# Optimization experiments

Hardware: AMD Instinct MI355X
Metric: run time of the kernel (lower is better)

Reference implementation:

```python
import jax, jax.numpy as jnp
import numpy as np

VOCAB = 12149
EMB = 50
TAGS = 9
HID = 128
START = 7
B, T = 256, 512


def setup_inputs() -> dict:
    key = jax.random.key(0)
    ks = jax.random.split(key, 12)
    s = 0.05
    return {
        "inputs": jax.random.randint(ks[0], (B, T), 0, VOCAB),
        "seq_label": jax.random.randint(ks[1], (B, T), 0, TAGS),
        "emb": jax.random.normal(ks[2], (VOCAB, EMB), jnp.float32) * s,
        "enc_Wx": jax.random.normal(ks[3], (EMB, HID), jnp.float32) * s,
        "enc_Wh": jax.random.normal(ks[4], (HID, HID), jnp.float32) * s,
        "enc_b": jnp.zeros((HID,), jnp.float32),
        "dec_emb": jax.random.normal(ks[5], (TAGS, EMB), jnp.float32) * s,
        "dec_Wx": jax.random.normal(ks[6], (EMB, HID), jnp.float32) * s,
        "dec_Wh": jax.random.normal(ks[7], (HID, HID), jnp.float32) * s,
        "dec_b": jnp.zeros((HID,), jnp.float32),
        "W": jax.random.normal(ks[8], (HID, TAGS), jnp.float32) * s,
        "b": jnp.zeros((TAGS,), jnp.float32),
    }


def _rnn(x_tbd, h0, Wx, Wh, b, collect):
    # x_tbd: [T, B, E]; SimpleRNN cell: h_t = tanh(x_t Wx + h_{t-1} Wh + b)
    def step(h, xt):
        h = jnp.tanh(xt @ Wx + h @ Wh + b)
        return h, (h if collect else None)
    hT, hs = jax.lax.scan(step, h0, x_tbd)
    return hT, hs


def reference(inputs, seq_label, emb, enc_Wx, enc_Wh, enc_b,
              dec_emb, dec_Wx, dec_Wh, dec_b, W, b):
    Bsz = inputs.shape[0]
    h0 = jnp.zeros((Bsz, HID), jnp.float32)
    # Encoder: only the final state is used as the decoder's initial state
    x = emb[inputs]                                  # [B, T, EMB]
    state, _ = _rnn(jnp.swapaxes(x, 0, 1), h0, enc_Wx, enc_Wh, enc_b, False)
    # Teacher forcing: prepend START token, drop last label
    dec_in = jnp.concatenate(
        [jnp.full((Bsz, 1), START, seq_label.dtype), seq_label], axis=1)[:, :-1]
    dx = dec_emb[dec_in]                             # [B, T, EMB]
    _, hs = _rnn(jnp.swapaxes(dx, 0, 1), state, dec_Wx, dec_Wh, dec_b, True)
    hs = jnp.swapaxes(hs, 0, 1)                      # [B, T, HID]
    return hs @ W + b                                # [B, T, TAGS]
```

## Files before the change

### kernel.cpp

```cpp
#include <hip/hip_runtime.h>
#include <hip/hip_bf16.h>

#define VOCAB 12149
#define EMB 50
#define TAGS 9
#define HID 128
#define START_TOK 7
#define BSZ 256
#define TLEN 512

typedef float v2f __attribute__((ext_vector_type(2)));

__device__ __forceinline__ float tanh_fast(float x) {
  float e = __expf(2.0f * x);
  return 1.0f - 2.0f * __builtin_amdgcn_rcpf(e + 1.0f);
}

template<int CTRL>
__device__ __forceinline__ float dpp_mov(float x) {
  return __int_as_float(__builtin_amdgcn_update_dpp(
      0, __float_as_int(x), CTRL, 0xF, 0xF, true));
}
template<int CTRL>
__device__ __forceinline__ v2f dpp2(v2f x) {
  v2f r;
  r.x = dpp_mov<CTRL>(x.x);
  r.y = dpp_mov<CTRL>(x.y);
  return r;
}
#define DPP_XOR1 0xB1
#define DPP_XOR2 0x4E
#define DPP_ROR4 0x124
#define DPP_ROR8 0x128
#define DPP_HALF_MIRROR 0x141
#define DPP_MIRROR 0x140

__global__ __launch_bounds__(128) void exw_kernel(
    const float* __restrict__ emb, const float* __restrict__ Wx,
    const float* __restrict__ bv, float* __restrict__ exw)
{
  __shared__ float wx_s[EMB * HID];
  __shared__ float emb_s[8 * EMB];
  const int tid = threadIdx.x;
  const int v0 = blockIdx.x * 8;
  for (int idx = tid; idx < EMB * HID; idx += 128) wx_s[idx] = Wx[idx];
  for (int idx = tid; idx < 8 * EMB; idx += 128) {
    int r = idx / EMB;
    int e = idx - r * EMB;
    int v = v0 + r;
    emb_s[idx] = (v < VOCAB) ? emb[v * EMB + e] : 0.0f;
  }
  __syncthreads();
  const float bj = bv[tid];
  for (int r = 0; r < 8; ++r) {
    int v = v0 + r;
    if (v >= VOCAB) break;
    float acc = bj;
#pragma unroll
    for (int e = 0; e < EMB; ++e) acc += emb_s[r * EMB + e] * wx_s[e * HID + tid];
    exw[v * HID + tid] = acc;
  }
}

__device__ __forceinline__ void dot_step(const float4 hA, const float4 hB,
                                         const v2f* __restrict__ wv, v2f acc[4]) {
  const float ha[4] = {hA.x, hA.y, hA.z, hA.w};
  const float hb[4] = {hB.x, hB.y, hB.z, hB.w};
#pragma unroll
  for (int c = 0; c < 4; ++c) {
    v2f h2 = {ha[c], ha[c]};
#pragma unroll
    for (int m = 0; m < 4; ++m)
      acc[m] = __builtin_elementwise_fma(h2, wv[c * 4 + m], acc[m]);
  }
#pragma unroll
  for (int c = 0; c < 4; ++c) {
    v2f h2 = {hb[c], hb[c]};
#pragma unroll
    for (int m = 0; m < 4; ++m)
      acc[m] = __builtin_elementwise_fma(h2, wv[16 + c * 4 + m], acc[m]);
  }
}

__global__ __launch_bounds__(256) void rnn_kernel(
    const int* __restrict__ inputs, const int* __restrict__ labels,
    const float* __restrict__ exw,
    const float* __restrict__ encWh,
    const float* __restrict__ dembG, const float* __restrict__ decWx,
    const float* __restrict__ decWh, const float* __restrict__ decb,
    const float* __restrict__ W, const float* __restrict__ bout,
    float* __restrict__ out)
{
  __shared__ __align__(16) float h_s[2][HID];
  __shared__ __align__(16) float dxw_s[TAGS * HID];
  __shared__ int tok_s[TLEN];
  __shared__ int lab_s[TLEN];
  __shared__ float demb_s[TAGS * EMB];

  const int i = threadIdx.x;
  const int w = i >> 6;
  const int lane = i & 63;
  const int l = lane & 15;
  const int g = lane >> 4;
  const int q = l & 3;
  const int jb = w * 32 + g * 8;
  const int bidx = blockIdx.x;

  tok_s[i] = inputs[bidx * TLEN + i];
  tok_s[i + 256] = inputs[bidx * TLEN + 256 + i];
  lab_s[i] = labels[bidx * TLEN + i];
  lab_s[i + 256] = labels[bidx * TLEN + 256 + i];
  for (int idx = i; idx < TAGS * EMB; idx += 256) demb_s[idx] = dembG[idx];
  if (i < HID) h_s[0][i] = 0.0f;

  v2f wv[32];
#pragma unroll
  for (int s = 0; s < 2; ++s)
#pragma unroll
    for (int c = 0; c < 4; ++c)
#pragma unroll
      for (int m = 0; m < 4; ++m)
        wv[s * 16 + c * 4 + m] =
            *(const v2f*)&encWh[(s * 64 + 4 * l + c) * HID + jb + 2 * (m ^ q)];

  const int oo = i >> 4;
  const int part = i & 15;
  const int s0 = (part >> 2) & 1;
  float wp[8];
  float bo = 0.0f;
#pragma unroll
  for (int u = 0; u < 8; ++u) wp[u] = 0.0f;
  if (oo < TAGS) {
#pragma unroll
    for (int s = 0; s < 2; ++s)
#pragma unroll
      for (int c = 0; c < 4; ++c)
        wp[s * 4 + c] = W[(part * 8 + (s ^ s0) * 4 + c) * TAGS + oo];
    bo = bout[oo];
  }
  __syncthreads();

  for (int task = i; task < TAGS * HID; task += 256) {
    int tag = task >> 7;
    int j2 = task & 127;
    float acc = decb[j2];
#pragma unroll
    for (int e = 0; e < EMB; ++e) acc += demb_s[tag * EMB + e] * decWx[e * HID + j2];
    dxw_s[task] = acc;
  }
  __syncthreads();

  const float* exw_q = exw + jb + 2 * q;
  int cur = 0;

  v2f xv0 = *(const v2f*)&exw_q[tok_s[0] * HID];
  v2f xv1 = *(const v2f*)&exw_q[tok_s[1] * HID];
  v2f xv2 = *(const v2f*)&exw_q[tok_s[2] * HID];
  v2f xv3 = *(const v2f*)&exw_q[tok_s[3] * HID];

#pragma unroll 4
  for (int t = 0; t < TLEN; ++t) {
    int tn = (t + 4 < TLEN) ? t + 4 : TLEN - 1;
    v2f xvn = *(const v2f*)&exw_q[tok_s[tn] * HID];

    float4 hA = *(const float4*)&h_s[cur][4 * l];
    float4 hB = *(const float4*)&h_s[cur][64 + 4 * l];
    v2f acc[4] = {v2f{0.f, 0.f}, v2f{0.f, 0.f}, v2f{0.f, 0.f}, v2f{0.f, 0.f}};
    dot_step(hA, hB, wv, acc);

    acc[0] += dpp2<DPP_XOR1>(acc[1]);
    acc[2] += dpp2<DPP_XOR1>(acc[3]);
    acc[0] += dpp2<DPP_XOR2>(acc[2]);
    acc[0] += dpp2<DPP_ROR4>(acc[0]);
    acc[0] += dpp2<DPP_ROR8>(acc[0]);

    v2f u = acc[0] + xv0;
    v2f hn;
    hn.x = tanh_fast(u.x);
    hn.y = tanh_fast(u.y);
    if (l < 4) *(v2f*)&h_s[cur ^ 1][jb + 2 * q] = hn;
    __syncthreads();
    cur ^= 1;
    xv0 = xv1; xv1 = xv2; xv2 = xv3; xv3 = xvn;
  }

#pragma unroll
  for (int s = 0; s < 2; ++s)
#pragma unroll
    for (int c = 0; c < 4; ++c)
#pragma unroll
      for (int m = 0; m < 4; ++m)
        wv[s * 16 + c * 4 + m] =
            *(const v2f*)&decWh[(s * 64 + 4 * l + c) * HID + jb + 2 * (m ^ q)];

#pragma unroll 2
  for (int t = 0; t < TLEN; ++t) {
    int lab = (t == 0) ? START_TOK : lab_s[t - 1];
    v2f xv = *(const v2f*)&dxw_s[lab * HID + jb + 2 * q];

    float4 hA = *(const float4*)&h_s[cur][4 * l];
    float4 hB = *(const float4*)&h_s[cur][64 + 4 * l];
    v2f acc[4] = {v2f{0.f, 0.f}, v2f{0.f, 0.f}, v2f{0.f, 0.f}, v2f{0.f, 0.f}};
    dot_step(hA, hB, wv, acc);

    acc[0] += dpp2<DPP_XOR1>(acc[1]);
    acc[2] += dpp2<DPP_XOR1>(acc[3]);
    acc[0] += dpp2<DPP_XOR2>(acc[2]);
    acc[0] += dpp2<DPP_ROR4>(acc[0]);
    acc[0] += dpp2<DPP_ROR8>(acc[0]);

    v2f u = acc[0] + xv;
    v2f hn;
    hn.x = tanh_fast(u.x);
    hn.y = tanh_fast(u.y);
    if (l < 4) *(v2f*)&h_s[cur ^ 1][jb + 2 * q] = hn;
    __syncthreads();
    cur ^= 1;

    if (oo < TAGS) {
      const float4* hp = (const float4*)(h_s[cur]) + part * 2;
      float pacc = 0.0f;
#pragma unroll
      for (int s = 0; s < 2; ++s) {
        float4 uu = hp[s ^ s0];
        pacc += uu.x * wp[s * 4 + 0]; pacc += uu.y * wp[s * 4 + 1];
        pacc += uu.z * wp[s * 4 + 2]; pacc += uu.w * wp[s * 4 + 3];
      }
      pacc += dpp_mov<DPP_XOR1>(pacc);
      pacc += dpp_mov<DPP_XOR2>(pacc);
      pacc += dpp_mov<DPP_HALF_MIRROR>(pacc);
      pacc += dpp_mov<DPP_MIRROR>(pacc);
      if (part == 0) out[(bidx * TLEN + t) * TAGS + oo] = pacc + bo;
    }
  }
}

extern "C" void kernel_launch(void* const* d_in, const int* in_sizes, int n_in,
                              void* d_out, int out_size, void* d_ws, size_t ws_size,
                              hipStream_t stream) {
  const int* inputs   = (const int*)d_in[0];
  const int* labels   = (const int*)d_in[1];
  const float* emb    = (const float*)d_in[2];
  const float* encWx  = (const float*)d_in[3];
  const float* encWh  = (const float*)d_in[4];
  const float* encb   = (const float*)d_in[5];
  const float* demb   = (const float*)d_in[6];
  const float* decWx  = (const float*)d_in[7];
  const float* decWh  = (const float*)d_in[8];
  const float* decb   = (const float*)d_in[9];
  const float* W      = (const float*)d_in[10];
  const float* bo     = (const float*)d_in[11];
  float* out = (float*)d_out;

  float* exw = (float*)d_ws;

  exw_kernel<<<(VOCAB + 7) / 8, 128, 0, stream>>>(emb, encWx, encb, exw);
  rnn_kernel<<<BSZ, 256, 0, stream>>>(inputs, labels, exw, encWh,
                                      demb, decWx, decWh, decb, W, bo, out);
}
```

Measured before the change: 400.5 us.

## Run recurrence in a single wavefront and offload output projection to a producer-consumer warp

The recurrence now runs entirely in one 64-lane wavefront, each lane owning two hidden units with the full 128x128 weight matrix held in registers. This removes the block-wide barrier each timestep and relies on wavefront lockstep execution to order the shared-memory reads and writes of h. The output projection moves to a second wavefront that consumes 64-step chunks from a double-buffered shared buffer, signalled through volatile flag and ack counters. The risks are heavy register pressure (256 floats of weights per lane), an implicit in-wave ordering assumption for h_s with no barrier, and spin-wait coordination between the two wavefronts.

Result: slower. 1.536 ms (+283.4%).

```diff
diff --git a/kernel.cpp b/kernel.cpp
--- a/kernel.cpp
+++ b/kernel.cpp
@@ -8,6 +8,8 @@
 #define START_TOK 7
 #define BSZ 256
 #define TLEN 512
+#define CH 64
+#define HPAD 132
 
 typedef float v2f __attribute__((ext_vector_type(2)));
 
@@ -30,10 +32,6 @@
 }
 #define DPP_XOR1 0xB1
 #define DPP_XOR2 0x4E
-#define DPP_ROR4 0x124
-#define DPP_ROR8 0x128
-#define DPP_HALF_MIRROR 0x141
-#define DPP_MIRROR 0x140
 
 __global__ __launch_bounds__(128) void exw_kernel(
     const float* __restrict__ emb, const float* __restrict__ Wx,
@@ -62,27 +60,36 @@
   }
 }
 
-__device__ __forceinline__ void dot_step(const float4 hA, const float4 hB,
-                                         const v2f* __restrict__ wv, v2f acc[4]) {
-  const float ha[4] = {hA.x, hA.y, hA.z, hA.w};
-  const float hb[4] = {hB.x, hB.y, hB.z, hB.w};
-#pragma unroll
-  for (int c = 0; c < 4; ++c) {
-    v2f h2 = {ha[c], ha[c]};
-#pragma unroll
-    for (int m = 0; m < 4; ++m)
-      acc[m] = __builtin_elementwise_fma(h2, wv[c * 4 + m], acc[m]);
-  }
-#pragma unroll
-  for (int c = 0; c < 4; ++c) {
-    v2f h2 = {hb[c], hb[c]};
-#pragma unroll
-    for (int m = 0; m < 4; ++m)
-      acc[m] = __builtin_elementwise_fma(h2, wv[16 + c * 4 + m], acc[m]);
-  }
-}
-
-__global__ __launch_bounds__(256) void rnn_kernel(
+__device__ __forceinline__ v2f rnn_dot(const float* __restrict__ h_s, int l2,
+                                       const v2f (&wL)[8][2][4],
+                                       const v2f (&wH)[8][2][4]) {
+  v2f aL[4], aH[4];
+#pragma unroll
+  for (int m = 0; m < 4; ++m) { aL[m] = v2f{0.f, 0.f}; aH[m] = v2f{0.f, 0.f}; }
+#pragma unroll
+  for (int r = 0; r < 8; ++r) {
+    const float4 hv = *(const float4*)&h_s[32 * l2 + 4 * ((r + 2 * l2) & 7)];
+    const v2f h2a = {hv.x, hv.y};
+    const v2f h2b = {hv.z, hv.w};
+#pragma unroll
+    for (int m = 0; m < 4; ++m) {
+      aL[m] = __builtin_elementwise_fma(h2a, wL[r][0][m], aL[m]);
+      aH[m] = __builtin_elementwise_fma(h2a, wH[r][0][m], aH[m]);
+      aL[m] = __builtin_elementwise_fma(h2b, wL[r][1][m], aL[m]);
+      aH[m] = __builtin_elementwise_fma(h2b, wH[r][1][m], aH[m]);
+    }
+  }
+  v2f u[4];
+#pragma unroll
+  for (int m = 0; m < 4; ++m)
+    u[m] = v2f{aL[m].x + aL[m].y, aH[m].x + aH[m].y};
+  u[0] += dpp2<DPP_XOR1>(u[1]);
+  u[2] += dpp2<DPP_XOR1>(u[3]);
+  u[0] += dpp2<DPP_XOR2>(u[2]);
+  return u[0];
+}
+
+__global__ __launch_bounds__(128, 1) void rnn_kernel(
     const int* __restrict__ inputs, const int* __restrict__ labels,
     const float* __restrict__ exw,
     const float* __restrict__ encWh,
@@ -91,146 +98,148 @@
     const float* __restrict__ W, const float* __restrict__ bout,
     float* __restrict__ out)
 {
-  __shared__ __align__(16) float h_s[2][HID];
+  __shared__ __align__(16) float h_s[HID];
   __shared__ __align__(16) float dxw_s[TAGS * HID];
+  __shared__ __align__(16) float Wt_s[TAGS][HID];
+  __shared__ __align__(16) float hchunk_s[2][CH][HPAD];
   __shared__ int tok_s[TLEN];
   __shared__ int lab_s[TLEN];
-  __shared__ float demb_s[TAGS * EMB];
-
-  const int i = threadIdx.x;
-  const int w = i >> 6;
-  const int lane = i & 63;
-  const int l = lane & 15;
-  const int g = lane >> 4;
-  const int q = l & 3;
-  const int jb = w * 32 + g * 8;
+  __shared__ int flag_s;
+  __shared__ int ack_s;
+
+  const int tid = threadIdx.x;
+  const int wid = tid >> 6;
+  const int lane = tid & 63;
   const int bidx = blockIdx.x;
 
-  tok_s[i] = inputs[bidx * TLEN + i];
-  tok_s[i + 256] = inputs[bidx * TLEN + 256 + i];
-  lab_s[i] = labels[bidx * TLEN + i];
-  lab_s[i + 256] = labels[bidx * TLEN + 256 + i];
-  for (int idx = i; idx < TAGS * EMB; idx += 256) demb_s[idx] = dembG[idx];
-  if (i < HID) h_s[0][i] = 0.0f;
-
-  v2f wv[32];
-#pragma unroll
-  for (int s = 0; s < 2; ++s)
-#pragma unroll
-    for (int c = 0; c < 4; ++c)
-#pragma unroll
-      for (int m = 0; m < 4; ++m)
-        wv[s * 16 + c * 4 + m] =
-            *(const v2f*)&encWh[(s * 64 + 4 * l + c) * HID + jb + 2 * (m ^ q)];
-
-  const int oo = i >> 4;
-  const int part = i & 15;
-  const int s0 = (part >> 2) & 1;
-  float wp[8];
-  float bo = 0.0f;
-#pragma unroll
-  for (int u = 0; u < 8; ++u) wp[u] = 0.0f;
-  if (oo < TAGS) {
-#pragma unroll
-    for (int s = 0; s < 2; ++s)
-#pragma unroll
-      for (int c = 0; c < 4; ++c)
-        wp[s * 4 + c] = W[(part * 8 + (s ^ s0) * 4 + c) * TAGS + oo];
-    bo = bout[oo];
-  }
+  for (int idx = tid; idx < TLEN; idx += 128) {
+    tok_s[idx] = inputs[bidx * TLEN + idx];
+    lab_s[idx] = labels[bidx * TLEN + idx];
+  }
+  for (int idx = tid; idx < TAGS * HID; idx += 128) {
+    int tag = idx >> 7;
+    int j2 = idx & 127;
+    float acc = decb[j2];
+#pragma unroll
+    for (int e = 0; e < EMB; ++e) acc += dembG[tag * EMB + e] * decWx[e * HID + j2];
+    dxw_s[idx] = acc;
+    Wt_s[tag][j2] = W[j2 * TAGS + tag];
+  }
+  if (tid < 64) { h_s[2 * tid] = 0.0f; h_s[2 * tid + 1] = 0.0f; }
+  if (tid == 0) { flag_s = 0; ack_s = 0; }
   __syncthreads();
 
-  for (int task = i; task < TAGS * HID; task += 256) {
-    int tag = task >> 7;
-    int j2 = task & 127;
-    float acc = decb[j2];
-#pragma unroll
-    for (int e = 0; e < EMB; ++e) acc += demb_s[tag * EMB + e] * decWx[e * HID + j2];
-    dxw_s[task] = acc;
-  }
-  __syncthreads();
-
-  const float* exw_q = exw + jb + 2 * q;
-  int cur = 0;
-
-  v2f xv0 = *(const v2f*)&exw_q[tok_s[0] * HID];
-  v2f xv1 = *(const v2f*)&exw_q[tok_s[1] * HID];
-  v2f xv2 = *(const v2f*)&exw_q[tok_s[2] * HID];
-  v2f xv3 = *(const v2f*)&exw_q[tok_s[3] * HID];
+  if (wid == 0) {
+    const int l2 = lane & 3;
+    const int jg = lane >> 2;
+
+    v2f wL[8][2][4], wH[8][2][4];
+#pragma unroll
+    for (int r = 0; r < 8; ++r) {
+      const int kb = 32 * l2 + 4 * ((r + 2 * l2) & 7);
+#pragma unroll
+      for (int p = 0; p < 2; ++p)
+#pragma unroll
+        for (int m = 0; m < 4; ++m) {
+          const int jlo = 8 * jg + 2 * (m ^ l2);
+          const int k0 = kb + 2 * p;
+          wL[r][p][m] = v2f{encWh[k0 * HID + jlo],     encWh[(k0 + 1) * HID + jlo]};
+          wH[r][p][m] = v2f{encWh[k0 * HID + jlo + 1], encWh[(k0 + 1) * HID + jlo + 1]};
+        }
+    }
+
+    const float* exw_q = exw + 2 * lane;
+    v2f xv0 = *(const v2f*)&exw_q[tok_s[0] * HID];
+    v2f xv1 = *(const v2f*)&exw_q[tok_s[1] * HID];
+    v2f xv2 = *(const v2f*)&exw_q[tok_s[2] * HID];
+    v2f xv3 = *(const v2f*)&exw_q[tok_s[3] * HID];
 
 #pragma unroll 4
-  for (int t = 0; t < TLEN; ++t) {
-    int tn = (t + 4 < TLEN) ? t + 4 : TLEN - 1;
-    v2f xvn = *(const v2f*)&exw_q[tok_s[tn] * HID];
-
-    float4 hA = *(const float4*)&h_s[cur][4 * l];
-    float4 hB = *(const float4*)&h_s[cur][64 + 4 * l];
-    v2f acc[4] = {v2f{0.f, 0.f}, v2f{0.f, 0.f}, v2f{0.f, 0.f}, v2f{0.f, 0.f}};
-    dot_step(hA, hB, wv, acc);
-
-    acc[0] += dpp2<DPP_XOR1>(acc[1]);
-    acc[2] += dpp2<DPP_XOR1>(acc[3]);
-    acc[0] += dpp2<DPP_XOR2>(acc[2]);
-    acc[0] += dpp2<DPP_ROR4>(acc[0]);
-    acc[0] += dpp2<DPP_ROR8>(acc[0]);
-
-    v2f u = acc[0] + xv0;
-    v2f hn;
-    hn.x = tanh_fast(u.x);
-    hn.y = tanh_fast(u.y);
-    if (l < 4) *(v2f*)&h_s[cur ^ 1][jb + 2 * q] = hn;
-    __syncthreads();
-    cur ^= 1;
-    xv0 = xv1; xv1 = xv2; xv2 = xv3; xv3 = xvn;
-  }
-
-#pragma unroll
-  for (int s = 0; s < 2; ++s)
-#pragma unroll
-    for (int c = 0; c < 4; ++c)
-#pragma unroll
-      for (int m = 0; m < 4; ++m)
-        wv[s * 16 + c * 4 + m] =
-            *(const v2f*)&decWh[(s * 64 + 4 * l + c) * HID + jb + 2 * (m ^ q)];
-
-#pragma unroll 2
-  for (int t = 0; t < TLEN; ++t) {
-    int lab = (t == 0) ? START_TOK : lab_s[t - 1];
-    v2f xv = *(const v2f*)&dxw_s[lab * HID + jb + 2 * q];
-
-    float4 hA = *(const float4*)&h_s[cur][4 * l];
-    float4 hB = *(const float4*)&h_s[cur][64 + 4 * l];
-    v2f acc[4] = {v2f{0.f, 0.f}, v2f{0.f, 0.f}, v2f{0.f, 0.f}, v2f{0.f, 0.f}};
-    dot_step(hA, hB, wv, acc);
-
-    acc[0] += dpp2<DPP_XOR1>(acc[1]);
-    acc[2] += dpp2<DPP_XOR1>(acc[3]);
-    acc[0] += dpp2<DPP_XOR2>(acc[2]);
-    acc[0] += dpp2<DPP_ROR4>(acc[0]);
-    acc[0] += dpp2<DPP_ROR8>(acc[0]);
-
-    v2f u = acc[0] + xv;
-    v2f hn;
-    hn.x = tanh_fast(u.x);
-    hn.y = tanh_fast(u.y);
-    if (l < 4) *(v2f*)&h_s[cur ^ 1][jb + 2 * q] = hn;
-    __syncthreads();
-    cur ^= 1;
-
-    if (oo < TAGS) {
-      const float4* hp = (const float4*)(h_s[cur]) + part * 2;
-      float pacc = 0.0f;
-#pragma unroll
-      for (int s = 0; s < 2; ++s) {
-        float4 uu = hp[s ^ s0];
-        pacc += uu.x * wp[s * 4 + 0]; pacc += uu.y * wp[s * 4 + 1];
-        pacc += uu.z * wp[s * 4 + 2]; pacc += uu.w * wp[s * 4 + 3];
+    for (int t = 0; t < TLEN; ++t) {
+      int tn = (t + 4 < TLEN) ? t + 4 : TLEN - 1;
+      v2f xvn = *(const v2f*)&exw_q[tok_s[tn] * HID];
+      v2f u = rnn_dot(h_s, l2, wL, wH) + xv0;
+      v2f hn;
+      hn.x = tanh_fast(u.x);
+      hn.y = tanh_fast(u.y);
+      *(v2f*)&h_s[2 * lane] = hn;
+      xv0 = xv1; xv1 = xv2; xv2 = xv3; xv3 = xvn;
+    }
+
+#pragma unroll
+    for (int r = 0; r < 8; ++r) {
+      const int kb = 32 * l2 + 4 * ((r + 2 * l2) & 7);
+#pragma unroll
+      for (int p = 0; p < 2; ++p)
+#pragma unroll
+        for (int m = 0; m < 4; ++m) {
+          const int jlo = 8 * jg + 2 * (m ^ l2);
+          const int k0 = kb + 2 * p;
+          wL[r][p][m] = v2f{decWh[k0 * HID + jlo],     decWh[(k0 + 1) * HID + jlo]};
+          wH[r][p][m] = v2f{decWh[k0 * HID + jlo + 1], decWh[(k0 + 1) * HID + jlo + 1]};
+        }
+    }
+
+#pragma unroll 4
+    for (int t = 0; t < TLEN; ++t) {
+      if ((t & (CH - 1)) == 0) {
+        int c = t >> 6;
+        if (c >= 2) {
+          while (*(volatile int*)&ack_s < c - 1) __builtin_amdgcn_s_sleep(2);
+          __asm volatile("" ::: "memory");
+        }
       }
-      pacc += dpp_mov<DPP_XOR1>(pacc);
-      pacc += dpp_mov<DPP_XOR2>(pacc);
-      pacc += dpp_mov<DPP_HALF_MIRROR>(pacc);
-      pacc += dpp_mov<DPP_MIRROR>(pacc);
-      if (part == 0) out[(bidx * TLEN + t) * TAGS + oo] = pacc + bo;
+      int lab = (t == 0) ? START_TOK : lab_s[t - 1];
+      v2f xv = *(const v2f*)&dxw_s[lab * HID + 2 * lane];
+      v2f u = rnn_dot(h_s, l2, wL, wH) + xv;
+      v2f hn;
+      hn.x = tanh_fast(u.x);
+      hn.y = tanh_fast(u.y);
+      *(v2f*)&h_s[2 * lane] = hn;
+      *(v2f*)&hchunk_s[(t >> 6) & 1][t & (CH - 1)][2 * lane] = hn;
+      if ((t & (CH - 1)) == CH - 1) {
+        __asm volatile("" ::: "memory");
+        if (lane == 0) *(volatile int*)&flag_s = (t >> 6) + 1;
+      }
+    }
+  } else {
+    float bb[TAGS];
+#pragma unroll
+    for (int o = 0; o < TAGS; ++o) bb[o] = bout[o];
+
+    for (int c = 0; c < TLEN / CH; ++c) {
+      while (*(volatile int*)&flag_s < c + 1) __builtin_amdgcn_s_sleep(8);
+      __asm volatile("" ::: "memory");
+      const float* hrow = &hchunk_s[c & 1][lane][0];
+      float oa[TAGS];
+#pragma unroll
+      for (int o = 0; o < TAGS; ++o) oa[o] = 0.0f;
+#pragma unroll
+      for (int hb = 0; hb < 2; ++hb) {
+        float4 hv[16];
+#pragma unroll
+        for (int c4 = 0; c4 < 16; ++c4)
+          hv[c4] = *(const float4*)&hrow[hb * 64 + 4 * c4];
+#pragma unroll
+        for (int o = 0; o < TAGS; ++o) {
+          v2f acc = {0.f, 0.f};
+#pragma unroll
+          for (int c4 = 0; c4 < 16; ++c4) {
+            const float4 wv4 = *(const float4*)&Wt_s[o][hb * 64 + 4 * c4];
+            acc = __builtin_elementwise_fma(v2f{hv[c4].x, hv[c4].y},
+                                            v2f{wv4.x, wv4.y}, acc);
+            acc = __builtin_elementwise_fma(v2f{hv[c4].z, hv[c4].w},
+                                            v2f{wv4.z, wv4.w}, acc);
+          }
+          oa[o] += acc.x + acc.y;
+        }
+      }
+      int t = c * CH + lane;
+      float* op = &out[(bidx * TLEN + t) * TAGS];
+#pragma unroll
+      for (int o = 0; o < TAGS; ++o) op[o] = oa[o] + bb[o];
+      __asm volatile("" ::: "memory");
+      if (lane == 0) *(volatile int*)&ack_s = c + 1;
     }
   }
 }
@@ -255,6 +264,6 @@
   float* exw = (float*)d_ws;
 
   exw_kernel<<<(VOCAB + 7) / 8, 128, 0, stream>>>(emb, encWx, encb, exw);
-  rnn_kernel<<<BSZ, 256, 0, stream>>>(inputs, labels, exw, encWh,
+  rnn_kernel<<<BSZ, 128, 0, stream>>>(inputs, labels, exw, encWh,
                                       demb, decWx, decWh, decb, W, bo, out);
 }
```
